# Kernel optimization log

Hardware: AMD Instinct MI355X
Metric: run time of the kernel (lower is better)

The kernel has to match this reference:

```python
import math
import jax, jax.numpy as jnp
import numpy as np

D_EMBD = 1024
N_HEAD = 16
BLOCK = 2048
B, T = 4, 2048


def setup_inputs() -> dict:
    key = jax.random.key(0)
    ks = jax.random.split(key, 5)
    d = D_EMBD
    return {
        "x": jax.random.normal(ks[0], (B, T, d), dtype=jnp.float32),
        "Wq": jax.random.normal(ks[1], (d, d), dtype=jnp.float32),
        "bq": jnp.zeros((d,), dtype=jnp.float32),
        "Wk": jax.random.normal(ks[2], (d, d), dtype=jnp.float32),
        "bk": jnp.zeros((d,), dtype=jnp.float32),
        "Wv": jax.random.normal(ks[3], (d, d), dtype=jnp.float32),
        "bv": jnp.zeros((d,), dtype=jnp.float32),
        "Wp": jax.random.normal(ks[4], (d, d), dtype=jnp.float32),
        "bp": jnp.zeros((d,), dtype=jnp.float32),
    }


def reference(x, Wq, bq, Wk, bk, Wv, bv, Wp, bp):
    Bb, Tt, C = x.shape
    n_head = N_HEAD
    hd = C // n_head  # head dim
    # QKV projections -> [B, H, T, hd]
    def split_heads(y):
        return y.reshape(Bb, Tt, n_head, hd).transpose(0, 2, 1, 3)
    Q = split_heads(x @ Wq + bq)
    K = split_heads(x @ Wk + bk)
    V = split_heads(x @ Wv + bv)
    # scores [B, H, T, T]
    attn = jnp.einsum('bhqd,bhkd->bhqk', Q, K) / math.sqrt(hd)
    # causal mask: -inf strictly above diagonal (matches triu(ones*-inf, 1))
    causal = jnp.tril(jnp.ones((Tt, Tt), dtype=bool))
    attn = jnp.where(causal, attn, -jnp.inf)
    attn = jax.nn.softmax(attn, axis=-1)
    y = jnp.einsum('bhqk,bhkd->bhqd', attn, V)
    y = y.transpose(0, 2, 1, 3).reshape(Bb, Tt, C)
    return y @ Wp + bp
```

## Files before the change

### kernel.cpp

```cpp
#include <hip/hip_runtime.h>
#include <stdint.h>
#include <stddef.h>

#define TT 2048
#define CC 1024
#define BBATCH 4
#define HH 16
#define HD 64
#define MTOT (BBATCH * TT)

typedef __bf16 bf16_t;
typedef __bf16 bf16x4 __attribute__((ext_vector_type(4)));
typedef __bf16 bf16x8 __attribute__((ext_vector_type(8)));
typedef float f32x4 __attribute__((ext_vector_type(4)));

typedef const __attribute__((address_space(1))) uint32_t* as1_u32p;
typedef __attribute__((address_space(3))) uint32_t* as3_u32p;

__device__ __forceinline__ f32x4 mfma16(bf16x8 a, bf16x8 b, f32x4 c) {
  return __builtin_amdgcn_mfma_f32_16x16x32_bf16(a, b, c, 0, 0, 0);
}

__device__ __forceinline__ void gload_lds16(void* lds, const void* g) {
  __builtin_amdgcn_global_load_lds((as1_u32p)g, (as3_u32p)lds, 16, 0, 0);
}

__device__ __forceinline__ bf16x8 rd32(const char* t, int row, int lane) {
  int sl = (lane >> 4) ^ ((row >> 1) & 3);
  return *(const bf16x8*)(t + row * 64 + sl * 16);
}
__device__ __forceinline__ bf16x8 rd64(const char* t, int row, int kk, int lane) {
  int sl = ((lane >> 4) + kk * 4) ^ (row & 7);
  return *(const bf16x8*)(t + row * 128 + sl * 16);
}

__global__ void split_x_kernel(const float* __restrict__ x, bf16_t* __restrict__ xh,
                               bf16_t* __restrict__ xl, int n4) {
  int stride = gridDim.x * blockDim.x;
  for (int i = blockIdx.x * blockDim.x + threadIdx.x; i < n4; i += stride) {
    float4 v = ((const float4*)x)[i];
    float vv[4] = {v.x, v.y, v.z, v.w};
    bf16x4 hv, lv;
#pragma unroll
    for (int j = 0; j < 4; ++j) {
      bf16_t h = (bf16_t)vv[j];
      hv[j] = h;
      lv[j] = (bf16_t)(vv[j] - (float)h);
    }
    *(bf16x4*)(xh + (size_t)i * 4) = hv;
    *(bf16x4*)(xl + (size_t)i * 4) = lv;
  }
}

__global__ void transpose_split_kernel(const float* __restrict__ Wq, const float* __restrict__ Wk,
                                       const float* __restrict__ Wv, const float* __restrict__ Wp,
                                       bf16_t* __restrict__ wqkh, bf16_t* __restrict__ wqkl,
                                       bf16_t* __restrict__ wv_t, bf16_t* __restrict__ wp_t) {
  __shared__ float tile[32][33];
  int mat = blockIdx.z;
  const float* W = (mat == 0) ? Wq : (mat == 1) ? Wk : (mat == 2) ? Wv : Wp;
  int tx = threadIdx.x, ty = threadIdx.y;
  int n0 = blockIdx.x * 32, k0 = blockIdx.y * 32;
#pragma unroll
  for (int j = 0; j < 32; j += 8)
    tile[ty + j][tx] = W[(size_t)(k0 + ty + j) * CC + n0 + tx];
  __syncthreads();
#pragma unroll
  for (int j = 0; j < 32; j += 8) {
    float v = tile[tx][ty + j];
    int n = n0 + ty + j, k = k0 + tx;
    if (mat <= 1) {
      bf16_t h = (bf16_t)v;
      size_t o = (size_t)(mat * CC + n) * CC + k;
      wqkh[o] = h;
      wqkl[o] = (bf16_t)(v - (float)h);
    } else {
      bf16_t* dst = (mat == 2) ? wv_t : wp_t;
      dst[(size_t)n * CC + k] = (bf16_t)v;
    }
  }
}

template <int MODE>
__global__ __launch_bounds__(256) void gemm_kernel(
    const bf16_t* __restrict__ Ah, const bf16_t* __restrict__ Al,
    const bf16_t* __restrict__ Bh, const bf16_t* __restrict__ Bl,
    const float* __restrict__ bias0, const float* __restrict__ bias1,
    void* __restrict__ out0, void* __restrict__ out1,
    void* __restrict__ out2, void* __restrict__ out3) {
  constexpr int NT = (MODE == 0) ? 4 : 2;
  __shared__ __align__(16) char smem[NT * 8192];
  char* sAh = smem;
  char* sAl = smem + 8192;
  char* sBh = smem + (MODE == 0 ? 16384 : 8192);
  char* sBl = smem + 24576;

  const int bn = blockIdx.x, bm = blockIdx.y;
  const int tid = threadIdx.x, w = tid >> 6, lane = tid & 63;
  const int wr = w >> 1, wc = w & 1;

  f32x4 acc[4][4] = {};

  for (int ks = 0; ks < 32; ++ks) {
    const int k0 = ks * 32;
    __syncthreads();
#pragma unroll
    for (int it = 0; it < 2; ++it) {
      int c = it * 4 + w;
      int row = c * 16 + (lane >> 2);
      int sl = (lane & 3) ^ ((row >> 1) & 3);
      size_t aoff = (size_t)(bm * 128 + row) * CC + k0 + sl * 8;
      size_t boff = (size_t)(bn * 128 + row) * CC + k0 + sl * 8;
      gload_lds16(sAh + c * 1024, Ah + aoff);
      gload_lds16(sBh + c * 1024, Bh + boff);
      if (MODE == 0) {
        gload_lds16(sAl + c * 1024, Al + aoff);
        gload_lds16(sBl + c * 1024, Bl + boff);
      }
    }
    __syncthreads();

    bf16x8 afh[4], bfh[4], afl[4], bfl[4];
#pragma unroll
    for (int i = 0; i < 4; ++i) {
      int ar = wr * 64 + i * 16 + (lane & 15);
      int br = wc * 64 + i * 16 + (lane & 15);
      afh[i] = rd32(sAh, ar, lane);
      bfh[i] = rd32(sBh, br, lane);
      if (MODE == 0) {
        afl[i] = rd32(sAl, ar, lane);
        bfl[i] = rd32(sBl, br, lane);
      }
    }
#pragma unroll
    for (int mi = 0; mi < 4; ++mi) {
#pragma unroll
      for (int ni = 0; ni < 4; ++ni) {
        acc[mi][ni] = mfma16(afh[mi], bfh[ni], acc[mi][ni]);
        if (MODE == 0) {
          acc[mi][ni] = mfma16(afh[mi], bfl[ni], acc[mi][ni]);
          acc[mi][ni] = mfma16(afl[mi], bfh[ni], acc[mi][ni]);
        }
      }
    }
  }

#pragma unroll
  for (int mi = 0; mi < 4; ++mi) {
#pragma unroll
    for (int ni = 0; ni < 4; ++ni) {
      const int col = bn * 128 + wc * 64 + ni * 16 + (lane & 15);
#pragma unroll
      for (int r = 0; r < 4; ++r) {
        const int row = bm * 128 + wr * 64 + mi * 16 + (lane >> 4) * 4 + r;
        float v = acc[mi][ni][r];
        if (MODE == 0) {
          const int which = col >> 10, c1 = col & 1023;
          const int h = c1 >> 6, d = c1 & 63;
          const int b = row >> 11, t = row & 2047;
          v += which ? bias1[c1] : bias0[c1];
          if (!which) v *= 0.125f;
          const size_t off = ((size_t)(b * HH + h) * TT + t) * HD + d;
          bf16_t hi = (bf16_t)v;
          bf16_t lo = (bf16_t)(v - (float)hi);
          ((bf16_t*)(which ? out2 : out0))[off] = hi;
          ((bf16_t*)(which ? out3 : out1))[off] = lo;
        } else if (MODE == 1) {
          const int h = col >> 6, d = col & 63;
          const int b = row >> 11, t = row & 2047;
          float vv = v + bias0[col];
          ((bf16_t*)out0)[((size_t)(b * HH + h) * HD + d) * TT + t] = (bf16_t)vv;
        } else {
          ((float*)out0)[(size_t)row * CC + col] = v + bias0[col];
        }
      }
    }
  }
}

__global__ __launch_bounds__(512, 4) void attn_kernel(
    const bf16_t* __restrict__ qh, const bf16_t* __restrict__ ql,
    const bf16_t* __restrict__ kh, const bf16_t* __restrict__ kl,
    const bf16_t* __restrict__ vt, bf16_t* __restrict__ y) {
  __shared__ __align__(16) char s_kh[2][8192];
  __shared__ __align__(16) char s_kl[2][8192];
  __shared__ __align__(16) char s_vt[2][8192];
  __shared__ __align__(16) char s_p[8][2048];

  const int blk = blockIdx.x;
  const int bh = (blk & 7) * 8 + ((blk >> 3) & 7);
  const int p = blk >> 6;
  const int b = bh >> 4, h = bh & 15;
  const int tid = threadIdx.x, w = tid >> 6, lane = tid & 63;
  const int hi = lane >> 4, qi = lane & 15;

  const int st_row = w * 8 + (lane >> 3);
  const int st_sl = (lane & 7) ^ (st_row & 7);
  const size_t st_koff0 = ((size_t)bh * TT + st_row) * HD + st_sl * 8;
  const size_t st_voff0 = ((size_t)bh * HD + st_row) * TT + st_sl * 8;

#pragma unroll
  for (int half = 0; half < 2; ++half) {
    const int qb = half ? (15 - p) : p;
    const int ktmax = 2 * qb + 1;
    const int qrow0 = qb * 128 + w * 16;
    const int qv = qrow0 + qi;

    bf16x8 qhf[2], qlf[2];
#pragma unroll
    for (int kk = 0; kk < 2; ++kk) {
      size_t off = ((size_t)bh * TT + qrow0 + qi) * HD + kk * 32 + hi * 8;
      qhf[kk] = *(const bf16x8*)(qh + off);
      qlf[kk] = *(const bf16x8*)(ql + off);
    }

    f32x4 o[4] = {};
    float m = -1e30f, l = 0.f;

    gload_lds16(s_kh[0] + w * 1024, kh + st_koff0);
    gload_lds16(s_kl[0] + w * 1024, kl + st_koff0);
    gload_lds16(s_vt[0] + w * 1024, vt + st_voff0);

    int cur = 0;
    for (int kt = 0; kt <= ktmax; ++kt) {
      if (kt < ktmax) {
        const size_t koff = st_koff0 + (size_t)(kt + 1) * 64 * HD;
        const size_t voff = st_voff0 + (size_t)(kt + 1) * 64;
        gload_lds16(s_kh[cur ^ 1] + w * 1024, kh + koff);
        gload_lds16(s_kl[cur ^ 1] + w * 1024, kl + koff);
        gload_lds16(s_vt[cur ^ 1] + w * 1024, vt + voff);
        asm volatile("s_waitcnt vmcnt(3)" ::: "memory");
      } else {
        asm volatile("s_waitcnt vmcnt(0)" ::: "memory");
      }
      __builtin_amdgcn_s_barrier();

      const char* ckh = s_kh[cur];
      const char* ckl = s_kl[cur];
      const char* cvt = s_vt[cur];
      const bool active = (qrow0 + 15 >= kt * 64);
      if (active) {
        f32x4 st[4];
#pragma unroll
        for (int cf = 0; cf < 4; ++cf) {
          f32x4 s = {};
#pragma unroll
          for (int kk = 0; kk < 2; ++kk) {
            bf16x8 kfh = rd64(ckh, cf * 16 + qi, kk, lane);
            bf16x8 kfl = rd64(ckl, cf * 16 + qi, kk, lane);
            s = mfma16(kfh, qhf[kk], s);
            s = mfma16(kfl, qhf[kk], s);
            s = mfma16(kfh, qlf[kk], s);
          }
          st[cf] = s;
        }

        if (kt * 64 + 63 > qrow0) {
#pragma unroll
          for (int cf = 0; cf < 4; ++cf)
#pragma unroll
            for (int r = 0; r < 4; ++r)
              if (kt * 64 + cf * 16 + hi * 4 + r > qv) st[cf][r] = -1e30f;
        }

        float tmax = st[0][0];
#pragma unroll
        for (int cf = 0; cf < 4; ++cf)
#pragma unroll
          for (int r = 0; r < 4; ++r) tmax = fmaxf(tmax, st[cf][r]);
        tmax = fmaxf(tmax, __shfl_xor(tmax, 16));
        tmax = fmaxf(tmax, __shfl_xor(tmax, 32));
        const float mnew = fmaxf(m, tmax);
        const float sc = __expf(m - mnew);
        float ps = 0.f;
#pragma unroll
        for (int cf = 0; cf < 4; ++cf) {
          bf16x4 pp;
#pragma unroll
          for (int r = 0; r < 4; ++r) {
            float pv = __expf(st[cf][r] - mnew);
            ps += pv;
            pp[r] = (bf16_t)pv;
          }
          int slot = ((cf << 1) + (hi >> 1)) ^ qi & 7;
          slot = ((cf << 1) + (hi >> 1)) ^ (qi & 7);
          *(bf16x4*)(&s_p[w][0] + qi * 128 + slot * 16 + (hi & 1) * 8) = pp;
        }
        ps += __shfl_xor(ps, 16);
        ps += __shfl_xor(ps, 32);
        l = l * sc + ps;
        m = mnew;
#pragma unroll
        for (int cd = 0; cd < 4; ++cd) {
#pragma unroll
          for (int r = 0; r < 4; ++r) o[cd][r] *= sc;
        }

#pragma unroll
        for (int kk = 0; kk < 2; ++kk) {
          bf16x8 pf = rd64(&s_p[w][0], qi, kk, lane);
#pragma unroll
          for (int cd = 0; cd < 4; ++cd) {
            bf16x8 vf = rd64(cvt, cd * 16 + qi, kk, lane);
            o[cd] = mfma16(vf, pf, o[cd]);
          }
        }
      }

      asm volatile("s_waitcnt lgkmcnt(0)" ::: "memory");
      __builtin_amdgcn_s_barrier();
      cur ^= 1;
    }

    const float inv = 1.f / l;
    const int t = qrow0 + qi;
#pragma unroll
    for (int cd = 0; cd < 4; ++cd) {
      bf16x4 ov;
#pragma unroll
      for (int r = 0; r < 4; ++r) ov[r] = (bf16_t)(o[cd][r] * inv);
      *(bf16x4*)(y + (size_t)(b * TT + t) * CC + h * HD + cd * 16 + hi * 4) = ov;
    }
  }
}

extern "C" void kernel_launch(void* const* d_in, const int* in_sizes, int n_in,
                              void* d_out, int out_size, void* d_ws, size_t ws_size,
                              hipStream_t stream) {
  (void)in_sizes; (void)n_in; (void)out_size; (void)ws_size;
  const float* x  = (const float*)d_in[0];
  const float* Wq = (const float*)d_in[1];
  const float* bq = (const float*)d_in[2];
  const float* Wk = (const float*)d_in[3];
  const float* bk = (const float*)d_in[4];
  const float* Wv = (const float*)d_in[5];
  const float* bv = (const float*)d_in[6];
  const float* Wp = (const float*)d_in[7];
  const float* bp = (const float*)d_in[8];

  char* ws = (char*)d_ws;
  const size_t MB = 1024 * 1024;
  bf16_t* xh   = (bf16_t*)(ws + 0 * MB);
  bf16_t* xl   = (bf16_t*)(ws + 16 * MB);
  bf16_t* wqkh = (bf16_t*)(ws + 32 * MB);
  bf16_t* wqkl = (bf16_t*)(ws + 36 * MB);
  bf16_t* wv_t = (bf16_t*)(ws + 40 * MB);
  bf16_t* wp_t = (bf16_t*)(ws + 42 * MB);
  bf16_t* qhw  = (bf16_t*)(ws + 44 * MB);
  bf16_t* qlw  = (bf16_t*)(ws + 60 * MB);
  bf16_t* khw  = (bf16_t*)(ws + 76 * MB);
  bf16_t* klw  = (bf16_t*)(ws + 92 * MB);
  bf16_t* vtw  = (bf16_t*)(ws + 108 * MB);
  bf16_t* yw   = (bf16_t*)(ws + 124 * MB);

  split_x_kernel<<<2048, 256, 0, stream>>>(x, xh, xl, MTOT * CC / 4);
  transpose_split_kernel<<<dim3(32, 32, 4), dim3(32, 8), 0, stream>>>(
      Wq, Wk, Wv, Wp, wqkh, wqkl, wv_t, wp_t);
  gemm_kernel<0><<<dim3(16, 64), 256, 0, stream>>>(
      xh, xl, wqkh, wqkl, bq, bk, qhw, qlw, khw, klw);
  gemm_kernel<1><<<dim3(8, 64), 256, 0, stream>>>(
      xh, nullptr, wv_t, nullptr, bv, nullptr, vtw, nullptr, nullptr, nullptr);
  attn_kernel<<<512, 512, 0, stream>>>(qhw, qlw, khw, klw, vtw, yw);
  gemm_kernel<2><<<dim3(8, 64), 256, 0, stream>>>(
      yw, nullptr, wp_t, nullptr, bp, nullptr, d_out, nullptr, nullptr, nullptr);
}
```

Measured before the change: 257.3 us.

## Add double-buffered 256x256 split-bf16 QK projection GEMM kernel

Moves the Q/K projection out of the generic templated GEMM into a dedicated kernel. It uses 512 threads, 256x256 output tiles and double-buffered LDS filled by direct global-to-LDS loads, with a partial vmcnt wait so the next K-slice loads while the current one is multiplied. The aim is to hide load latency and raise data reuse per tile for the three-MFMA hi/lo split product. In exchange it needs 128KB of LDS and a large accumulator array per wave, so occupancy is lower, and the grid shrinks to 256 blocks.

```diff
diff --git a/kernel.cpp b/kernel.cpp
--- a/kernel.cpp
+++ b/kernel.cpp
@@ -81,19 +81,121 @@
   }
 }
 
+__global__ __launch_bounds__(512, 2) void gemm_qk_kernel(
+    const bf16_t* __restrict__ Ah, const bf16_t* __restrict__ Al,
+    const bf16_t* __restrict__ Bh, const bf16_t* __restrict__ Bl,
+    const float* __restrict__ bq, const float* __restrict__ bk,
+    bf16_t* __restrict__ qh, bf16_t* __restrict__ ql,
+    bf16_t* __restrict__ kh, bf16_t* __restrict__ kl) {
+  __shared__ __align__(16) char s_ah[2][16384];
+  __shared__ __align__(16) char s_al[2][16384];
+  __shared__ __align__(16) char s_bh[2][16384];
+  __shared__ __align__(16) char s_bl[2][16384];
+
+  const int blk = blockIdx.x;
+  const int bn = blk & 7;
+  const int bm = blk >> 3;
+  const int tid = threadIdx.x, w = tid >> 6, lane = tid & 63;
+  const int wr = w >> 2, wc = w & 3;
+  const int qi = lane & 15, hi = lane >> 4;
+
+  const int c0 = w * 2, c1 = w * 2 + 1;
+  const int srow0 = c0 * 16 + (lane >> 2);
+  const int srow1 = c1 * 16 + (lane >> 2);
+  const int ssl0 = (lane & 3) ^ ((srow0 >> 1) & 3);
+  const int ssl1 = (lane & 3) ^ ((srow1 >> 1) & 3);
+  const size_t a_off0 = (size_t)(bm * 256 + srow0) * CC + ssl0 * 8;
+  const size_t a_off1 = (size_t)(bm * 256 + srow1) * CC + ssl1 * 8;
+  const size_t b_off0 = (size_t)(bn * 256 + srow0) * CC + ssl0 * 8;
+  const size_t b_off1 = (size_t)(bn * 256 + srow1) * CC + ssl1 * 8;
+
+  f32x4 acc[8][4] = {};
+
+#define STAGE_QK(buf, k0)                                        \
+  do {                                                           \
+    gload_lds16(s_ah[buf] + c0 * 1024, Ah + a_off0 + (k0));      \
+    gload_lds16(s_ah[buf] + c1 * 1024, Ah + a_off1 + (k0));      \
+    gload_lds16(s_al[buf] + c0 * 1024, Al + a_off0 + (k0));      \
+    gload_lds16(s_al[buf] + c1 * 1024, Al + a_off1 + (k0));      \
+    gload_lds16(s_bh[buf] + c0 * 1024, Bh + b_off0 + (k0));      \
+    gload_lds16(s_bh[buf] + c1 * 1024, Bh + b_off1 + (k0));      \
+    gload_lds16(s_bl[buf] + c0 * 1024, Bl + b_off0 + (k0));      \
+    gload_lds16(s_bl[buf] + c1 * 1024, Bl + b_off1 + (k0));      \
+  } while (0)
+
+  STAGE_QK(0, 0);
+  int cur = 0;
+  for (int ks = 0; ks < 32; ++ks) {
+    if (ks < 31) {
+      STAGE_QK(cur ^ 1, (ks + 1) * 32);
+      asm volatile("s_waitcnt vmcnt(8)" ::: "memory");
+    } else {
+      asm volatile("s_waitcnt vmcnt(0)" ::: "memory");
+    }
+    __builtin_amdgcn_s_barrier();
+
+    bf16x8 bfh[4], bfl[4];
+#pragma unroll
+    for (int ni = 0; ni < 4; ++ni) {
+      int br = wc * 64 + ni * 16 + qi;
+      bfh[ni] = rd32(s_bh[cur], br, lane);
+      bfl[ni] = rd32(s_bl[cur], br, lane);
+    }
+    __builtin_amdgcn_s_setprio(1);
+#pragma unroll
+    for (int mi = 0; mi < 8; ++mi) {
+      int ar = wr * 128 + mi * 16 + qi;
+      bf16x8 ahf = rd32(s_ah[cur], ar, lane);
+      bf16x8 alf = rd32(s_al[cur], ar, lane);
+#pragma unroll
+      for (int ni = 0; ni < 4; ++ni) {
+        acc[mi][ni] = mfma16(ahf, bfh[ni], acc[mi][ni]);
+        acc[mi][ni] = mfma16(ahf, bfl[ni], acc[mi][ni]);
+        acc[mi][ni] = mfma16(alf, bfh[ni], acc[mi][ni]);
+      }
+    }
+    __builtin_amdgcn_s_setprio(0);
+    asm volatile("s_waitcnt lgkmcnt(0)" ::: "memory");
+    __builtin_amdgcn_s_barrier();
+    cur ^= 1;
+  }
+#undef STAGE_QK
+
+  const int which = bn >> 2;
+  const float* bias = which ? bk : bq;
+  bf16_t* oh = which ? kh : qh;
+  bf16_t* ol = which ? kl : ql;
+#pragma unroll
+  for (int mi = 0; mi < 8; ++mi) {
+#pragma unroll
+    for (int ni = 0; ni < 4; ++ni) {
+      const int col = bn * 256 + wc * 64 + ni * 16 + qi;
+      const int c1i = col & 1023;
+      const int h = c1i >> 6, d = c1i & 63;
+#pragma unroll
+      for (int r = 0; r < 4; ++r) {
+        const int row = bm * 256 + wr * 128 + mi * 16 + hi * 4 + r;
+        const int b = row >> 11, t = row & 2047;
+        float v = acc[mi][ni][r] + bias[c1i];
+        if (!which) v *= 0.125f;
+        const size_t off = ((size_t)(b * HH + h) * TT + t) * HD + d;
+        bf16_t hv = (bf16_t)v;
+        oh[off] = hv;
+        ol[off] = (bf16_t)(v - (float)hv);
+      }
+    }
+  }
+}
+
 template <int MODE>
 __global__ __launch_bounds__(256) void gemm_kernel(
-    const bf16_t* __restrict__ Ah, const bf16_t* __restrict__ Al,
-    const bf16_t* __restrict__ Bh, const bf16_t* __restrict__ Bl,
-    const float* __restrict__ bias0, const float* __restrict__ bias1,
-    void* __restrict__ out0, void* __restrict__ out1,
-    void* __restrict__ out2, void* __restrict__ out3) {
-  constexpr int NT = (MODE == 0) ? 4 : 2;
-  __shared__ __align__(16) char smem[NT * 8192];
+    const bf16_t* __restrict__ Ah,
+    const bf16_t* __restrict__ Bh,
+    const float* __restrict__ bias0,
+    void* __restrict__ out0) {
+  __shared__ __align__(16) char smem[2 * 8192];
   char* sAh = smem;
-  char* sAl = smem + 8192;
-  char* sBh = smem + (MODE == 0 ? 16384 : 8192);
-  char* sBl = smem + 24576;
+  char* sBh = smem + 8192;
 
   const int bn = blockIdx.x, bm = blockIdx.y;
   const int tid = threadIdx.x, w = tid >> 6, lane = tid & 63;
@@ -113,34 +215,22 @@
       size_t boff = (size_t)(bn * 128 + row) * CC + k0 + sl * 8;
       gload_lds16(sAh + c * 1024, Ah + aoff);
       gload_lds16(sBh + c * 1024, Bh + boff);
-      if (MODE == 0) {
-        gload_lds16(sAl + c * 1024, Al + aoff);
-        gload_lds16(sBl + c * 1024, Bl + boff);
-      }
     }
     __syncthreads();
 
-    bf16x8 afh[4], bfh[4], afl[4], bfl[4];
+    bf16x8 afh[4], bfh[4];
 #pragma unroll
     for (int i = 0; i < 4; ++i) {
       int ar = wr * 64 + i * 16 + (lane & 15);
       int br = wc * 64 + i * 16 + (lane & 15);
       afh[i] = rd32(sAh, ar, lane);
       bfh[i] = rd32(sBh, br, lane);
-      if (MODE == 0) {
-        afl[i] = rd32(sAl, ar, lane);
-        bfl[i] = rd32(sBl, br, lane);
-      }
     }
 #pragma unroll
     for (int mi = 0; mi < 4; ++mi) {
 #pragma unroll
       for (int ni = 0; ni < 4; ++ni) {
         acc[mi][ni] = mfma16(afh[mi], bfh[ni], acc[mi][ni]);
-        if (MODE == 0) {
-          acc[mi][ni] = mfma16(afh[mi], bfl[ni], acc[mi][ni]);
-          acc[mi][ni] = mfma16(afl[mi], bfh[ni], acc[mi][ni]);
-        }
       }
     }
   }
@@ -154,18 +244,7 @@
       for (int r = 0; r < 4; ++r) {
         const int row = bm * 128 + wr * 64 + mi * 16 + (lane >> 4) * 4 + r;
         float v = acc[mi][ni][r];
-        if (MODE == 0) {
-          const int which = col >> 10, c1 = col & 1023;
-          const int h = c1 >> 6, d = c1 & 63;
-          const int b = row >> 11, t = row & 2047;
-          v += which ? bias1[c1] : bias0[c1];
-          if (!which) v *= 0.125f;
-          const size_t off = ((size_t)(b * HH + h) * TT + t) * HD + d;
-          bf16_t hi = (bf16_t)v;
-          bf16_t lo = (bf16_t)(v - (float)hi);
-          ((bf16_t*)(which ? out2 : out0))[off] = hi;
-          ((bf16_t*)(which ? out3 : out1))[off] = lo;
-        } else if (MODE == 1) {
+        if (MODE == 1) {
           const int h = col >> 6, d = col & 63;
           const int b = row >> 11, t = row & 2047;
           float vv = v + bias0[col];
@@ -282,8 +361,7 @@
             ps += pv;
             pp[r] = (bf16_t)pv;
           }
-          int slot = ((cf << 1) + (hi >> 1)) ^ qi & 7;
-          slot = ((cf << 1) + (hi >> 1)) ^ (qi & 7);
+          int slot = ((cf << 1) + (hi >> 1)) ^ (qi & 7);
           *(bf16x4*)(&s_p[w][0] + qi * 128 + slot * 16 + (hi & 1) * 8) = pp;
         }
         ps += __shfl_xor(ps, 16);
@@ -356,11 +434,11 @@
   split_x_kernel<<<2048, 256, 0, stream>>>(x, xh, xl, MTOT * CC / 4);
   transpose_split_kernel<<<dim3(32, 32, 4), dim3(32, 8), 0, stream>>>(
       Wq, Wk, Wv, Wp, wqkh, wqkl, wv_t, wp_t);
-  gemm_kernel<0><<<dim3(16, 64), 256, 0, stream>>>(
+  gemm_qk_kernel<<<256, 512, 0, stream>>>(
       xh, xl, wqkh, wqkl, bq, bk, qhw, qlw, khw, klw);
   gemm_kernel<1><<<dim3(8, 64), 256, 0, stream>>>(
-      xh, nullptr, wv_t, nullptr, bv, nullptr, vtw, nullptr, nullptr, nullptr);
+      xh, wv_t, bv, vtw);
   attn_kernel<<<512, 512, 0, stream>>>(qhw, qlw, khw, klw, vtw, yw);
   gemm_kernel<2><<<dim3(8, 64), 256, 0, stream>>>(
-      yw, nullptr, wp_t, nullptr, bp, nullptr, d_out, nullptr, nullptr, nullptr);
-}
+      yw, wp_t, bp, d_out);
+}
```

Result: faster. 250.4 us (-2.7%).
